# Optimization experiments

Measured on AMD Instinct MI355X. Metric: run time of the kernel, lower is better.

Reference implementation:

```python
import jax, jax.numpy as jnp
import numpy as np

B, N_IN, N_OUT = 16, 7000, 28000
C_IN, C_OUT, S = 64, 64, 9
NNZ = 3 * N_OUT  # ~3 source verts per upsampled vert (barycentric)


def setup_inputs() -> dict:
    key = jax.random.key(0)
    k = jax.random.split(key, 6)
    x = jax.random.normal(k[0], (B, N_IN, C_IN), dtype=jnp.float32)
    values = jax.random.uniform(k[1], (NNZ,), dtype=jnp.float32)
    row = jax.random.randint(k[2], (NNZ,), 0, N_OUT)
    col = jax.random.randint(k[3], (NNZ,), 0, N_IN)
    spiral_indices = jax.random.randint(k[4], (N_OUT, S), 0, N_OUT)
    weight = jax.random.normal(k[5], (S * C_IN, C_OUT), dtype=jnp.float32) * 0.02
    bias = jnp.zeros((C_OUT,), dtype=jnp.float32)
    return {"x": x, "values": values, "weight": weight, "bias": bias,
            "row": row, "col": col, "spiral_indices": spiral_indices}


def reference(x, values, weight, bias, row, col, spiral_indices):
    # Pool: gather source verts, scale by sparse matrix values, scatter-add to output verts
    n_out = spiral_indices.shape[0]
    gathered = x[:, col, :] * values[None, :, None]            # [B, nnz, C]
    pooled = jnp.zeros((x.shape[0], n_out, x.shape[2]), x.dtype).at[:, row, :].add(gathered)  # [B, N_out, C]
    # SpiralConv: gather spiral neighborhood, flatten, linear
    feat = pooled[:, spiral_indices.reshape(-1), :]            # [B, N_out*S, C]
    feat = feat.reshape(x.shape[0], n_out, -1)                 # [B, N_out, S*C]
    out = jax.nn.elu(jnp.einsum('bnf,fo->bno', feat, weight) + bias)
    return out
```

## Files before the change

### kernel.cpp

```cpp
#include <hip/hip_runtime.h>
#include <math.h>

#define B      16
#define N_IN   7000
#define N_OUT  28000
#define C      64
#define S      9
#define NNZ    (3 * N_OUT)
#define F      (S * C)
#define KB     (F / 32)

typedef short bf16x8 __attribute__((ext_vector_type(8)));
typedef float f32x4  __attribute__((ext_vector_type(4)));

static __device__ __forceinline__ unsigned short f2bf(float f) {
    unsigned u = __float_as_uint(f);
    u += 0x7fffu + ((u >> 16) & 1u);
    return (unsigned short)(u >> 16);
}
static __device__ __forceinline__ float bf2f(unsigned short s) {
    return __uint_as_float((unsigned)s << 16);
}

__global__ void hist_kernel(const int* __restrict__ row, int* __restrict__ cnt) {
    int i = blockIdx.x * 256 + threadIdx.x;
    if (i < NNZ) atomicAdd(&cnt[row[i]], 1);
}

__global__ void scan_kernel(const int* __restrict__ cnt,
                            int* __restrict__ offs, int* __restrict__ cursor) {
    __shared__ int tmp[1024];
    const int t = threadIdx.x;
    const int base = t * 28;
    const bool live = (t < 1000);

    int c[28];
    int partial = 0;
    if (live) {
        #pragma unroll
        for (int j = 0; j < 28; ++j) { c[j] = cnt[base + j]; partial += c[j]; }
    }
    tmp[t] = partial;
    __syncthreads();
    #pragma unroll
    for (int off = 1; off < 1024; off <<= 1) {
        int v = (t >= off) ? tmp[t - off] : 0;
        __syncthreads();
        tmp[t] += v;
        __syncthreads();
    }
    if (live) {
        int run = tmp[t] - partial;
        #pragma unroll
        for (int j = 0; j < 28; ++j) {
            offs[base + j]   = run;
            cursor[base + j] = run;
            run += c[j];
        }
        if (t == 999) offs[N_OUT] = run;
    }
}

__global__ void place_kernel(const int* __restrict__ row, const int* __restrict__ col,
                             const float* __restrict__ values,
                             int* __restrict__ cursor,
                             int* __restrict__ ecol, float* __restrict__ eval) {
    int i = blockIdx.x * 256 + threadIdx.x;
    if (i < NNZ) {
        int pos = atomicAdd(&cursor[row[i]], 1);
        ecol[pos] = col[i];
        eval[pos] = values[i];
    }
}

__global__ void xbf_kernel(const float* __restrict__ x, unsigned short* __restrict__ xb) {
    const size_t i = ((size_t)blockIdx.x * 256 + threadIdx.x) * 8;
    const float4 a = *(const float4*)(x + i);
    const float4 c = *(const float4*)(x + i + 4);
    ushort4 o0, o1;
    o0.x = f2bf(a.x); o0.y = f2bf(a.y); o0.z = f2bf(a.z); o0.w = f2bf(a.w);
    o1.x = f2bf(c.x); o1.y = f2bf(c.y); o1.z = f2bf(c.z); o1.w = f2bf(c.w);
    *(ushort4*)(xb + i)     = o0;
    *(ushort4*)(xb + i + 4) = o1;
}

__global__ void pool_kernel(const unsigned short* __restrict__ xb,
                            const int*   __restrict__ ecol,
                            const float* __restrict__ eval,
                            const int*   __restrict__ offs,
                            unsigned short* __restrict__ pooled) {
    const int bg     = blockIdx.x & 7;
    const int rowblk = blockIdx.x >> 3;
    const int wave = threadIdx.x >> 6;
    const int lane = threadIdx.x & 63;
    const int rsub = lane >> 5;
    const int bsub = (lane >> 4) & 1;
    const int sl   = lane & 15;

    const int r = rowblk * 8 + wave * 2 + rsub;
    const int b = bg + 8 * bsub;

    const int start = offs[r], end = offs[r + 1];

    float4 acc = make_float4(0.f, 0.f, 0.f, 0.f);
    const unsigned short* xbb = xb + (size_t)b * N_IN * C + sl * 4;

    for (int e = start; e < end; e += 4) {
        const int nn = end - e;
        int   cl[4]; float vv[4];
        #pragma unroll
        for (int j = 0; j < 4; ++j) {
            const int ee = (j < nn) ? e + j : e;
            cl[j] = ecol[ee];
            vv[j] = (j < nn) ? eval[ee] : 0.f;
        }
        ushort4 xv[4];
        #pragma unroll
        for (int j = 0; j < 4; ++j)
            xv[j] = *(const ushort4*)(xbb + (size_t)cl[j] * C);
        #pragma unroll
        for (int j = 0; j < 4; ++j) {
            acc.x = fmaf(bf2f(xv[j].x), vv[j], acc.x);
            acc.y = fmaf(bf2f(xv[j].y), vv[j], acc.y);
            acc.z = fmaf(bf2f(xv[j].z), vv[j], acc.z);
            acc.w = fmaf(bf2f(xv[j].w), vv[j], acc.w);
        }
    }

    unsigned long long ov =
        (unsigned long long)f2bf(acc.x)
        | ((unsigned long long)f2bf(acc.y) << 16)
        | ((unsigned long long)f2bf(acc.z) << 32)
        | ((unsigned long long)f2bf(acc.w) << 48);
    unsigned short* dst = pooled + (size_t)bsub * (N_OUT * 512)
                        + (size_t)r * 512 + bg * 64 + sl * 4;
    __builtin_nontemporal_store(ov, (unsigned long long*)dst);
}

__global__ void packw_kernel(const float* __restrict__ w, unsigned short* __restrict__ pw) {
    const int kb   = blockIdx.x;
    const int nt   = threadIdx.x >> 6;
    const int lane = threadIdx.x & 63;
    const int lm   = lane & 15;
    const int quad = lane >> 4;

    unsigned short v[8];
    #pragma unroll
    for (int j = 0; j < 8; ++j) {
        const int k = kb * 32 + quad * 8 + j;
        const int n = nt * 16 + lm;
        v[j] = f2bf(w[(size_t)k * C + n]);
    }
    unsigned short* dst = pw + ((size_t)(kb * 4 + nt) * 64 + lane) * 8;
    #pragma unroll
    for (int j = 0; j < 8; ++j) dst[j] = v[j];
}

__global__ __launch_bounds__(512, 4)
void spiral_mfma(const unsigned short* __restrict__ pooled,
                 const bf16x8*         __restrict__ packedW,
                 const int*            __restrict__ sp,
                 const float*          __restrict__ bias,
                 float*                __restrict__ out) {
    const int Lb    = blockIdx.x;
    const int g     = Lb & 1;
    const int mtile = Lb >> 1;
    const int tid   = threadIdx.x;
    const int wave  = tid >> 6;
    const int lane  = tid & 63;
    const int lm    = lane & 15;
    const int quad  = lane >> 4;
    const int m_base = mtile * 32;
    const int b      = g * 8 + wave;

    __shared__ unsigned short apool[2][32][512];
    __shared__ bf16x8         bstage[2][512];

    int spv[S];
    {
        const int r = m_base + (lane & 31);
        #pragma unroll
        for (int s = 0; s < S; ++s) spv[s] = sp[r * S + s];
    }

    const unsigned short* pgbase = pooled + (size_t)g * (N_OUT * 512);

    f32x4 acc[2][4];
    #pragma unroll
    for (int t = 0; t < 2; ++t)
        #pragma unroll
        for (int nt = 0; nt < 4; ++nt)
            acc[t][nt] = (f32x4){0.f, 0.f, 0.f, 0.f};

    bf16x8 ldA[4];
    bf16x8 ldB;

    #pragma unroll
    for (int q = 0; q < 4; ++q) {
        const int r = __shfl(spv[0], wave * 4 + q, 64);
        ldA[q] = *(const bf16x8*)(pgbase + (size_t)r * 512 + lane * 8);
    }
    ldB = packedW[tid];
    #pragma unroll
    for (int q = 0; q < 4; ++q) {
        const int j = wave * 4 + q;
        *(bf16x8*)(&apool[0][j][(lane ^ (j & 7)) * 8]) = ldA[q];
    }
    bstage[0][tid] = ldB;
    __syncthreads();

    #pragma unroll
    for (int s = 0; s < S; ++s) {
        const int cur = s & 1, nxt = cur ^ 1;

        if (s + 1 < S) {
            #pragma unroll
            for (int q = 0; q < 4; ++q) {
                const int r = __shfl(spv[s + 1], wave * 4 + q, 64);
                ldA[q] = *(const bf16x8*)(pgbase + (size_t)r * 512 + lane * 8);
            }
            ldB = packedW[(s + 1) * 512 + tid];
        }

        #pragma unroll
        for (int half = 0; half < 2; ++half) {
            bf16x8 bb[4];
            #pragma unroll
            for (int nt = 0; nt < 4; ++nt)
                bb[nt] = bstage[cur][(half * 4 + nt) * 64 + lane];
            bf16x8 aa[2];
            #pragma unroll
            for (int t = 0; t < 2; ++t) {
                const int j = t * 16 + lm;
                const int chunk = wave * 8 + (((half * 4 + quad) ^ (j & 7)));
                aa[t] = *(const bf16x8*)(&apool[cur][j][chunk * 8]);
            }
            #pragma unroll
            for (int nt = 0; nt < 4; ++nt)
                #pragma unroll
                for (int t = 0; t < 2; ++t)
                    acc[t][nt] = __builtin_amdgcn_mfma_f32_16x16x32_bf16(
                        aa[t], bb[nt], acc[t][nt], 0, 0, 0);
        }

        if (s + 1 < S) {
            #pragma unroll
            for (int q = 0; q < 4; ++q) {
                const int j = wave * 4 + q;
                *(bf16x8*)(&apool[nxt][j][(lane ^ (j & 7)) * 8]) = ldA[q];
            }
            bstage[nxt][tid] = ldB;
        }
        __syncthreads();
    }

    #pragma unroll
    for (int nt = 0; nt < 4; ++nt) {
        const int n = nt * 16 + lm;
        const float bs = bias[n];
        #pragma unroll
        for (int t = 0; t < 2; ++t) {
            #pragma unroll
            for (int reg = 0; reg < 4; ++reg) {
                const int r = m_base + t * 16 + quad * 4 + reg;
                float v = acc[t][nt][reg] + bs;
                v = v > 0.f ? v : (__expf(v) - 1.0f);
                __builtin_nontemporal_store(v,
                    out + ((size_t)b * N_OUT + r) * C + n);
            }
        }
    }
}

extern "C" void kernel_launch(void* const* d_in, const int* in_sizes, int n_in,
                              void* d_out, int out_size, void* d_ws, size_t ws_size,
                              hipStream_t stream) {
    const float* x      = (const float*)d_in[0];
    const float* values = (const float*)d_in[1];
    const float* weight = (const float*)d_in[2];
    const float* bias   = (const float*)d_in[3];
    const int*   row    = (const int*)d_in[4];
    const int*   col    = (const int*)d_in[5];
    const int*   sp     = (const int*)d_in[6];
    float*       out    = (float*)d_out;

    char* ws = (char*)d_ws;
    size_t off = 0;
    unsigned short* pooled  = (unsigned short*)(ws + off); off += (size_t)B * N_OUT * C * 2;
    unsigned short* packedW = (unsigned short*)(ws + off); off += (size_t)KB * 4 * 64 * 8 * 2;
    unsigned short* xbf     = (unsigned short*)(ws + off); off += (size_t)B * N_IN * C * 2;
    int*   offs   = (int*)(ws + off); off += ((size_t)(N_OUT + 1) * 4 + 124) / 128 * 128;
    int*   cursor = (int*)(ws + off); off += (size_t)N_OUT * 4 + 128;
    int*   cnt    = (int*)(ws + off); off += (size_t)N_OUT * 4 + 128;
    int*   ecol   = (int*)(ws + off); off += (size_t)NNZ * 4;
    float* eval   = (float*)(ws + off); off += (size_t)NNZ * 4;

    (void)hipMemsetAsync(cnt, 0, (size_t)N_OUT * 4, stream);
    hist_kernel <<<(NNZ + 255) / 256, 256, 0, stream>>>(row, cnt);
    scan_kernel <<<1, 1024, 0, stream>>>(cnt, offs, cursor);
    place_kernel<<<(NNZ + 255) / 256, 256, 0, stream>>>(row, col, values, cursor, ecol, eval);

    packw_kernel<<<KB, 256, 0, stream>>>(weight, packedW);

    xbf_kernel<<<3500, 256, 0, stream>>>(x, xbf);

    pool_kernel<<<3500 * 8, 256, 0, stream>>>(xbf, ecol, eval, offs, pooled);

    spiral_mfma<<<875 * 2, 512, 0, stream>>>(pooled,
        reinterpret_cast<const bf16x8*>(packedW), sp, bias, out);
}
```

Before: 296.3 us.

## Merge prep kernels, rewrite scan with wave shuffles, deepen spiral prefetch

Fuses the bf16 conversion of x, the row histogram and the weight packing into one prep kernel to cut launch overhead. Rewrites the single-block prefix scan as a chunked wave-shuffle scan with a carried total. In the spiral MFMA kernel, global loads are prefetched two steps ahead using double register buffers, and __syncthreads is replaced by a barrier that waits only on LDS traffic so global loads stay in flight across it. This costs extra registers, which may reduce occupancy, and the lighter barrier depends on the compiler still inserting vmcnt waits before the buffered loads are used.

```diff
diff --git a/kernel.cpp b/kernel.cpp
--- a/kernel.cpp
+++ b/kernel.cpp
@@ -22,43 +22,77 @@
     return __uint_as_float((unsigned)s << 16);
 }
 
-__global__ void hist_kernel(const int* __restrict__ row, int* __restrict__ cnt) {
-    int i = blockIdx.x * 256 + threadIdx.x;
-    if (i < NNZ) atomicAdd(&cnt[row[i]], 1);
+#define XBF_BLOCKS  3500
+#define HIST_BLOCKS 329
+#define PACK_BLOCKS 18
+
+__global__ void prep_kernel(const float* __restrict__ x, unsigned short* __restrict__ xb,
+                            const float* __restrict__ w, unsigned short* __restrict__ pw,
+                            const int*   __restrict__ row, int* __restrict__ cnt) {
+    const int blk = blockIdx.x;
+    const int tid = threadIdx.x;
+    if (blk < XBF_BLOCKS) {
+        const size_t i = ((size_t)blk * 256 + tid) * 8;
+        const float4 a = *(const float4*)(x + i);
+        const float4 c = *(const float4*)(x + i + 4);
+        ushort4 o0, o1;
+        o0.x = f2bf(a.x); o0.y = f2bf(a.y); o0.z = f2bf(a.z); o0.w = f2bf(a.w);
+        o1.x = f2bf(c.x); o1.y = f2bf(c.y); o1.z = f2bf(c.z); o1.w = f2bf(c.w);
+        *(ushort4*)(xb + i)     = o0;
+        *(ushort4*)(xb + i + 4) = o1;
+    } else if (blk < XBF_BLOCKS + HIST_BLOCKS) {
+        const int i = (blk - XBF_BLOCKS) * 256 + tid;
+        if (i < NNZ) atomicAdd(&cnt[row[i]], 1);
+    } else {
+        const int kb   = blk - (XBF_BLOCKS + HIST_BLOCKS);
+        const int nt   = tid >> 6;
+        const int lane = tid & 63;
+        const int lm   = lane & 15;
+        const int quad = lane >> 4;
+        unsigned short v[8];
+        #pragma unroll
+        for (int j = 0; j < 8; ++j) {
+            const int k = kb * 32 + quad * 8 + j;
+            const int n = nt * 16 + lm;
+            v[j] = f2bf(w[(size_t)k * C + n]);
+        }
+        unsigned short* dst = pw + ((size_t)(kb * 4 + nt) * 64 + lane) * 8;
+        #pragma unroll
+        for (int j = 0; j < 8; ++j) dst[j] = v[j];
+    }
 }
 
 __global__ void scan_kernel(const int* __restrict__ cnt,
                             int* __restrict__ offs, int* __restrict__ cursor) {
-    __shared__ int tmp[1024];
-    const int t = threadIdx.x;
-    const int base = t * 28;
-    const bool live = (t < 1000);
-
-    int c[28];
-    int partial = 0;
-    if (live) {
-        #pragma unroll
-        for (int j = 0; j < 28; ++j) { c[j] = cnt[base + j]; partial += c[j]; }
-    }
-    tmp[t] = partial;
+    __shared__ int wsum[16];
+    __shared__ int carry;
+    const int t = threadIdx.x, lane = t & 63, wid = t >> 6;
+    if (t == 0) carry = 0;
     __syncthreads();
-    #pragma unroll
-    for (int off = 1; off < 1024; off <<= 1) {
-        int v = (t >= off) ? tmp[t - off] : 0;
+    int lastTot = 0;
+    #pragma unroll 1
+    for (int chunk = 0; chunk < 28; ++chunk) {
+        const int idx = chunk * 1024 + t;
+        const int v = (idx < N_OUT) ? cnt[idx] : 0;
+        const int cin = carry;
+        int sc = v;
+        #pragma unroll
+        for (int d = 1; d < 64; d <<= 1) {
+            int u = __shfl_up(sc, d, 64);
+            if (lane >= d) sc += u;
+        }
+        if (lane == 63) wsum[wid] = sc;
         __syncthreads();
-        tmp[t] += v;
+        int wexcl = 0;
+        #pragma unroll
+        for (int wj = 0; wj < 15; ++wj)
+            wexcl += (wj < wid) ? wsum[wj] : 0;
+        const int excl = cin + wexcl + sc - v;
+        if (idx < N_OUT) { offs[idx] = excl; cursor[idx] = excl; }
+        if (t == 1023) { lastTot = cin + wexcl + sc; carry = lastTot; }
         __syncthreads();
     }
-    if (live) {
-        int run = tmp[t] - partial;
-        #pragma unroll
-        for (int j = 0; j < 28; ++j) {
-            offs[base + j]   = run;
-            cursor[base + j] = run;
-            run += c[j];
-        }
-        if (t == 999) offs[N_OUT] = run;
-    }
+    if (t == 1023) offs[N_OUT] = lastTot;
 }
 
 __global__ void place_kernel(const int* __restrict__ row, const int* __restrict__ col,
@@ -71,17 +105,6 @@
         ecol[pos] = col[i];
         eval[pos] = values[i];
     }
-}
-
-__global__ void xbf_kernel(const float* __restrict__ x, unsigned short* __restrict__ xb) {
-    const size_t i = ((size_t)blockIdx.x * 256 + threadIdx.x) * 8;
-    const float4 a = *(const float4*)(x + i);
-    const float4 c = *(const float4*)(x + i + 4);
-    ushort4 o0, o1;
-    o0.x = f2bf(a.x); o0.y = f2bf(a.y); o0.z = f2bf(a.z); o0.w = f2bf(a.w);
-    o1.x = f2bf(c.x); o1.y = f2bf(c.y); o1.z = f2bf(c.z); o1.w = f2bf(c.w);
-    *(ushort4*)(xb + i)     = o0;
-    *(ushort4*)(xb + i + 4) = o1;
 }
 
 __global__ void pool_kernel(const unsigned short* __restrict__ xb,
@@ -137,24 +160,10 @@
     __builtin_nontemporal_store(ov, (unsigned long long*)dst);
 }
 
-__global__ void packw_kernel(const float* __restrict__ w, unsigned short* __restrict__ pw) {
-    const int kb   = blockIdx.x;
-    const int nt   = threadIdx.x >> 6;
-    const int lane = threadIdx.x & 63;
-    const int lm   = lane & 15;
-    const int quad = lane >> 4;
-
-    unsigned short v[8];
-    #pragma unroll
-    for (int j = 0; j < 8; ++j) {
-        const int k = kb * 32 + quad * 8 + j;
-        const int n = nt * 16 + lm;
-        v[j] = f2bf(w[(size_t)k * C + n]);
-    }
-    unsigned short* dst = pw + ((size_t)(kb * 4 + nt) * 64 + lane) * 8;
-    #pragma unroll
-    for (int j = 0; j < 8; ++j) dst[j] = v[j];
-}
+#define BARRIER_NODRAIN() do {                                   \
+    asm volatile("s_waitcnt lgkmcnt(0)" ::: "memory");           \
+    __builtin_amdgcn_s_barrier();                                \
+} while (0)
 
 __global__ __launch_bounds__(512, 4)
 void spiral_mfma(const unsigned short* __restrict__ pooled,
@@ -192,34 +201,40 @@
         for (int nt = 0; nt < 4; ++nt)
             acc[t][nt] = (f32x4){0.f, 0.f, 0.f, 0.f};
 
-    bf16x8 ldA[4];
-    bf16x8 ldB;
+    bf16x8 ldA2[2][4];
+    bf16x8 ldB2[2];
 
     #pragma unroll
     for (int q = 0; q < 4; ++q) {
         const int r = __shfl(spv[0], wave * 4 + q, 64);
-        ldA[q] = *(const bf16x8*)(pgbase + (size_t)r * 512 + lane * 8);
-    }
-    ldB = packedW[tid];
+        ldA2[0][q] = *(const bf16x8*)(pgbase + (size_t)r * 512 + lane * 8);
+    }
+    ldB2[0] = packedW[tid];
+    #pragma unroll
+    for (int q = 0; q < 4; ++q) {
+        const int r = __shfl(spv[1], wave * 4 + q, 64);
+        ldA2[1][q] = *(const bf16x8*)(pgbase + (size_t)r * 512 + lane * 8);
+    }
+    ldB2[1] = packedW[512 + tid];
     #pragma unroll
     for (int q = 0; q < 4; ++q) {
         const int j = wave * 4 + q;
-        *(bf16x8*)(&apool[0][j][(lane ^ (j & 7)) * 8]) = ldA[q];
-    }
-    bstage[0][tid] = ldB;
-    __syncthreads();
+        *(bf16x8*)(&apool[0][j][(lane ^ (j & 7)) * 8]) = ldA2[0][q];
+    }
+    bstage[0][tid] = ldB2[0];
+    BARRIER_NODRAIN();
 
     #pragma unroll
     for (int s = 0; s < S; ++s) {
         const int cur = s & 1, nxt = cur ^ 1;
 
-        if (s + 1 < S) {
+        if (s + 2 < S) {
             #pragma unroll
             for (int q = 0; q < 4; ++q) {
-                const int r = __shfl(spv[s + 1], wave * 4 + q, 64);
-                ldA[q] = *(const bf16x8*)(pgbase + (size_t)r * 512 + lane * 8);
+                const int r = __shfl(spv[s + 2], wave * 4 + q, 64);
+                ldA2[s & 1][q] = *(const bf16x8*)(pgbase + (size_t)r * 512 + lane * 8);
             }
-            ldB = packedW[(s + 1) * 512 + tid];
+            ldB2[s & 1] = packedW[(s + 2) * 512 + tid];
         }
 
         #pragma unroll
@@ -247,11 +262,11 @@
             #pragma unroll
             for (int q = 0; q < 4; ++q) {
                 const int j = wave * 4 + q;
-                *(bf16x8*)(&apool[nxt][j][(lane ^ (j & 7)) * 8]) = ldA[q];
+                *(bf16x8*)(&apool[nxt][j][(lane ^ (j & 7)) * 8]) = ldA2[(s + 1) & 1][q];
             }
-            bstage[nxt][tid] = ldB;
-        }
-        __syncthreads();
+            bstage[nxt][tid] = ldB2[(s + 1) & 1];
+        }
+        BARRIER_NODRAIN();
     }
 
     #pragma unroll
@@ -296,13 +311,13 @@
     float* eval   = (float*)(ws + off); off += (size_t)NNZ * 4;
 
     (void)hipMemsetAsync(cnt, 0, (size_t)N_OUT * 4, stream);
-    hist_kernel <<<(NNZ + 255) / 256, 256, 0, stream>>>(row, cnt);
-    scan_kernel <<<1, 1024, 0, stream>>>(cnt, offs, cursor);
+
+    prep_kernel<<<XBF_BLOCKS + HIST_BLOCKS + PACK_BLOCKS, 256, 0, stream>>>(
+        x, xbf, weight, packedW, row, cnt);
+
+    scan_kernel<<<1, 1024, 0, stream>>>(cnt, offs, cursor);
+
     place_kernel<<<(NNZ + 255) / 256, 256, 0, stream>>>(row, col, values, cursor, ecol, eval);
-
-    packw_kernel<<<KB, 256, 0, stream>>>(weight, packedW);
-
-    xbf_kernel<<<3500, 256, 0, stream>>>(x, xbf);
 
     pool_kernel<<<3500 * 8, 256, 0, stream>>>(xbf, ecol, eval, offs, pooled);
 
```

Measured after the change: 303.2 us. 1.02x slower.
